# Kernel optimization log

Hardware: AMD Instinct MI355X
Metric: run time of the kernel (lower is better)

## Reference

```python
import jax, jax.numpy as jnp
import numpy as np

B, T, C, H, W = 16, 128, 32, 16, 16
NUM_FEAT = 16
D = C * H * W            # conv1d in-channels (kernel size 1 => linear)
G = NUM_FEAT * H * W     # G3 out-channels


def setup_inputs() -> dict:
    key = jax.random.key(0)
    ks = jax.random.split(key, 8)
    s1 = 1.0 / np.sqrt(D)
    return {
        "input1": jax.random.normal(ks[0], (B, T, C, H, W), jnp.float32),
        "input2": jax.random.normal(ks[1], (B, T, C, H, W), jnp.float32),
        "w1": jax.random.uniform(ks[2], (NUM_FEAT, D), jnp.float32, -s1, s1),
        "b1": jax.random.uniform(ks[3], (NUM_FEAT,), jnp.float32, -s1, s1),
        "w2": jax.random.uniform(ks[4], (NUM_FEAT, D), jnp.float32, -s1, s1),
        "b2": jax.random.uniform(ks[5], (NUM_FEAT,), jnp.float32, -s1, s1),
        "w3": jax.random.uniform(ks[6], (G, D), jnp.float32, -s1, s1),
        "b3": jax.random.uniform(ks[7], (G,), jnp.float32, -s1, s1),
    }


def reference(input1, input2, w1, b1, w2, b2, w3, b3):
    b, t = input1.shape[:2]
    x1 = input1.reshape(b, t, D)  # [B,T,D]
    x2 = input2.reshape(b, t, D)
    # Conv1d(kernel=1) projections (channels-first conv == per-frame linear)
    q = jnp.einsum('btd,fd->btf', x1, w1) + b1          # [B,T,F]
    k = jnp.einsum('bsd,fd->bsf', x2, w2) + b2          # [B,S,F]
    scores = jnp.einsum('btf,bsf->bts', q, k)            # [B,T,T]
    attn = jax.nn.softmax(scores, axis=1)                # softmax over dim=1 (rows)
    v = jnp.einsum('bsd,gd->bsg', x1, w3) + b3           # [B,T,G]
    out = jnp.einsum('bts,bsg->btg', attn, v)            # [B,T,G]
    return out.reshape(b, t, NUM_FEAT, H, W)
```

## Files before the change

### kernel.cpp

```cpp
#include <hip/hip_runtime.h>
#include <cstdint>
#include <cstddef>

#define Bn 16
#define Tn 128
#define Dn 8192
#define Fn 16
#define Gn 4096
#define MT (Bn*Tn)

typedef __attribute__((ext_vector_type(8))) short short8;
typedef __attribute__((ext_vector_type(4))) float f32x4;

__device__ inline short f2bf(float f) {
    union { float f; uint32_t u; } c; c.f = f;
    uint32_t u = c.u;
    uint32_t r = (u + 0x7FFFu + ((u >> 16) & 1u)) >> 16;
    return (short)(r & 0xFFFFu);
}

__device__ inline short8 cvt8(float4 a, float4 b) {
    short8 v;
    v[0] = f2bf(a.x); v[1] = f2bf(a.y); v[2] = f2bf(a.z); v[3] = f2bf(a.w);
    v[4] = f2bf(b.x); v[5] = f2bf(b.y); v[6] = f2bf(b.z); v[7] = f2bf(b.w);
    return v;
}

#define N8_X1 (MT * Dn / 8)
#define N8_W3 ((size_t)Gn * Dn / 8)

__global__ __launch_bounds__(256) void cvt2_kernel(
    const float* __restrict__ x1, const float* __restrict__ w3,
    short* __restrict__ x1b, short* __restrict__ w3b)
{
    const size_t total = N8_X1 + N8_W3;
    size_t i = (size_t)blockIdx.x * 256 + threadIdx.x;
    const size_t stride = (size_t)gridDim.x * 256;
    for (; i < total; i += stride) {
        if (i < N8_X1) {
            const float4* s = ((const float4*)x1) + i * 2;
            ((short8*)x1b)[i] = cvt8(s[0], s[1]);
        } else {
            const size_t j = i - N8_X1;
            const float4* s = ((const float4*)w3) + j * 2;
            ((short8*)w3b)[j] = cvt8(s[0], s[1]);
        }
    }
}

__global__ __launch_bounds__(256) void qk_gemm_kernel(
    const short* __restrict__ x1b, const float* __restrict__ x2,
    const float* __restrict__ w1, const float* __restrict__ w2,
    const float* __restrict__ b1, const float* __restrict__ b2,
    float* __restrict__ q, float* __restrict__ k)
{
    __shared__ float red[4][16][16];
    const int tid = threadIdx.x;
    const int tile = blockIdx.x >> 1;
    const int isK  = blockIdx.x & 1;
    const int m0 = tile * 16;
    const int wave = tid >> 6, lane = tid & 63;
    const int quad = lane >> 4, r = lane & 15;
    const int kbase = wave * (Dn / 4);

    f32x4 acc = {};

    if (!isK) {
        const short* ap = x1b + (size_t)(m0 + r) * Dn + kbase + quad * 8;
        const float* bp = w1 + (size_t)r * Dn + kbase + quad * 8;
        #pragma unroll 4
        for (int it = 0; it < 64; ++it) {
            short8 af = *(const short8*)(ap + it * 32);
            const float4* b4 = (const float4*)(bp + it * 32);
            short8 bf = cvt8(b4[0], b4[1]);
            acc = __builtin_amdgcn_mfma_f32_16x16x32_bf16(af, bf, acc, 0, 0, 0);
        }
    } else {
        const float* apf = x2 + (size_t)(m0 + r) * Dn + kbase + quad * 8;
        const float* bp  = w2 + (size_t)r * Dn + kbase + quad * 8;
        #pragma unroll 4
        for (int it = 0; it < 64; ++it) {
            const float4* a4 = (const float4*)(apf + it * 32);
            short8 af = cvt8(a4[0], a4[1]);
            const float4* b4 = (const float4*)(bp + it * 32);
            short8 bf = cvt8(b4[0], b4[1]);
            acc = __builtin_amdgcn_mfma_f32_16x16x32_bf16(af, bf, acc, 0, 0, 0);
        }
    }

    #pragma unroll
    for (int reg = 0; reg < 4; ++reg)
        red[wave][quad * 4 + reg][r] = acc[reg];
    __syncthreads();

    const int m = tid >> 4, f = tid & 15;
    float s = red[0][m][f] + red[1][m][f] + red[2][m][f] + red[3][m][f];
    s += (isK ? b2 : b1)[f];
    (isK ? k : q)[(m0 + m) * Fn + f] = s;
}

__global__ __launch_bounds__(128) void attn_kernel(
    const float* __restrict__ q, const float* __restrict__ k,
    short* __restrict__ attn16)
{
    __shared__ float qs[Tn * 17];
    const int b = blockIdx.x;
    const int tid = threadIdx.x;

    for (int i = tid; i < Tn * Fn; i += 128)
        qs[(i >> 4) * 17 + (i & 15)] = q[b * Tn * Fn + i];
    __syncthreads();

    float kr[16];
    #pragma unroll
    for (int f = 0; f < 16; ++f) kr[f] = k[b * Tn * Fn + tid * Fn + f];

    float m = -1e30f, sum = 0.f;
    #pragma unroll 1
    for (int t = 0; t < Tn; ++t) {
        float sc = 0.f;
        #pragma unroll
        for (int f = 0; f < 16; ++f) sc += qs[t * 17 + f] * kr[f];
        if (sc > m) { sum = sum * __expf(m - sc) + 1.f; m = sc; }
        else        { sum += __expf(sc - m); }
    }
    const float inv = 1.f / sum;
    short* ap = attn16 + (size_t)b * Tn * Tn;
    #pragma unroll 1
    for (int t = 0; t < Tn; ++t) {
        float sc = 0.f;
        #pragma unroll
        for (int f = 0; f < 16; ++f) sc += qs[t * 17 + f] * kr[f];
        ap[t * Tn + tid] = f2bf(__expf(sc - m) * inv);
    }
}

#define BK 32
#define KSPLIT 2
#define KHALF (Dn / KSPLIT)

__global__ __launch_bounds__(256) void gemm_v_split_kernel(
    const short* __restrict__ A, const short* __restrict__ Bw,
    float* __restrict__ vTf)
{
    __shared__ __attribute__((aligned(16))) short As[128 * BK];
    __shared__ __attribute__((aligned(16))) short Bs[128 * BK];

    const int tid = threadIdx.x;
    const int m0 = blockIdx.y * 128;
    const int n0 = blockIdx.x * 128;
    const int z  = blockIdx.z;
    const int kbase = z * KHALF;
    float* outp = vTf + (size_t)z * Gn * MT;
    const int wave = tid >> 6, lane = tid & 63;
    const int wm = (wave >> 1) * 64, wn = (wave & 1) * 64;
    const int quad = lane >> 4, r = lane & 15;

    const int srow = wave * 32 + (lane >> 2);
    const int scol = (lane & 3) * 8;
    const short* gA = A  + (size_t)(m0 + srow) * Dn + kbase + scol;
    const short* gB = Bw + (size_t)(n0 + srow) * Dn + kbase + scol;
    short* lA = &As[srow * BK + scol];
    short* lB = &Bs[srow * BK + scol];

    f32x4 acc[4][4] = {};

    #pragma unroll 1
    for (int k0 = 0; k0 < KHALF; k0 += BK) {
        __syncthreads();
        __builtin_amdgcn_global_load_lds(
            (const __attribute__((address_space(1))) void*)(gA + k0),
            (__attribute__((address_space(3))) void*)lA, 16, 0, 0);
        __builtin_amdgcn_global_load_lds(
            (const __attribute__((address_space(1))) void*)(gA + k0 + (size_t)16 * Dn),
            (__attribute__((address_space(3))) void*)(lA + 16 * BK), 16, 0, 0);
        __builtin_amdgcn_global_load_lds(
            (const __attribute__((address_space(1))) void*)(gB + k0),
            (__attribute__((address_space(3))) void*)lB, 16, 0, 0);
        __builtin_amdgcn_global_load_lds(
            (const __attribute__((address_space(1))) void*)(gB + k0 + (size_t)16 * Dn),
            (__attribute__((address_space(3))) void*)(lB + 16 * BK), 16, 0, 0);
        __syncthreads();

        short8 af[4], bf[4];
        #pragma unroll
        for (int i = 0; i < 4; ++i)
            af[i] = *(const short8*)&As[(wm + i * 16 + r) * BK + quad * 8];
        #pragma unroll
        for (int j = 0; j < 4; ++j)
            bf[j] = *(const short8*)&Bs[(wn + j * 16 + r) * BK + quad * 8];

        #pragma unroll
        for (int i = 0; i < 4; ++i)
            #pragma unroll
            for (int j = 0; j < 4; ++j)
                acc[i][j] = __builtin_amdgcn_mfma_f32_16x16x32_bf16(
                    af[i], bf[j], acc[i][j], 0, 0, 0);
    }

    #pragma unroll
    for (int i = 0; i < 4; ++i) {
        #pragma unroll
        for (int reg = 0; reg < 4; ++reg) {
            const int rowg = m0 + wm + i * 16 + quad * 4 + reg;
            #pragma unroll
            for (int j = 0; j < 4; ++j) {
                const int col = n0 + wn + j * 16 + r;
                outp[(size_t)rowg * MT + col] = acc[i][j][reg];
            }
        }
    }
}

__global__ __launch_bounds__(256) void vt_cvt_kernel(
    const float* __restrict__ vTf, const float* __restrict__ bias,
    short* __restrict__ vT)
{
    const size_t N8 = (size_t)Gn * MT / 8;
    const float4* p0 = (const float4*)vTf;
    const float4* p1 = (const float4*)(vTf + (size_t)Gn * MT);
    size_t i = (size_t)blockIdx.x * 256 + threadIdx.x;
    const size_t stride = (size_t)gridDim.x * 256;
    for (; i < N8; i += stride) {
        const float bv = bias[i >> 8];
        float4 a0 = p0[i * 2], b0 = p0[i * 2 + 1];
        float4 a1 = p1[i * 2], b1 = p1[i * 2 + 1];
        a0.x += a1.x + bv; a0.y += a1.y + bv; a0.z += a1.z + bv; a0.w += a1.w + bv;
        b0.x += b1.x + bv; b0.y += b1.y + bv; b0.z += b1.z + bv; b0.w += b1.w + bv;
        ((short8*)vT)[i] = cvt8(a0, b0);
    }
}

__global__ __launch_bounds__(256) void gemm_v_kernel(
    const short* __restrict__ A, const short* __restrict__ Bw,
    const float* __restrict__ bias, short* __restrict__ vT)
{
    __shared__ __attribute__((aligned(16))) short As[128 * BK];
    __shared__ __attribute__((aligned(16))) short Bs[128 * BK];

    const int tid = threadIdx.x;
    const int m0 = blockIdx.y * 128;
    const int n0 = blockIdx.x * 128;
    const int wave = tid >> 6, lane = tid & 63;
    const int wm = (wave >> 1) * 64, wn = (wave & 1) * 64;
    const int quad = lane >> 4, r = lane & 15;

    const int srow = wave * 32 + (lane >> 2);
    const int scol = (lane & 3) * 8;
    const short* gA = A  + (size_t)(m0 + srow) * Dn + scol;
    const short* gB = Bw + (size_t)(n0 + srow) * Dn + scol;
    short* lA = &As[srow * BK + scol];
    short* lB = &Bs[srow * BK + scol];

    f32x4 acc[4][4] = {};

    #pragma unroll 1
    for (int k0 = 0; k0 < Dn; k0 += BK) {
        __syncthreads();
        __builtin_amdgcn_global_load_lds(
            (const __attribute__((address_space(1))) void*)(gA + k0),
            (__attribute__((address_space(3))) void*)lA, 16, 0, 0);
        __builtin_amdgcn_global_load_lds(
            (const __attribute__((address_space(1))) void*)(gA + k0 + (size_t)16 * Dn),
            (__attribute__((address_space(3))) void*)(lA + 16 * BK), 16, 0, 0);
        __builtin_amdgcn_global_load_lds(
            (const __attribute__((address_space(1))) void*)(gB + k0),
            (__attribute__((address_space(3))) void*)lB, 16, 0, 0);
        __builtin_amdgcn_global_load_lds(
            (const __attribute__((address_space(1))) void*)(gB + k0 + (size_t)16 * Dn),
            (__attribute__((address_space(3))) void*)(lB + 16 * BK), 16, 0, 0);
        __syncthreads();

        short8 af[4], bf[4];
        #pragma unroll
        for (int i = 0; i < 4; ++i)
            af[i] = *(const short8*)&As[(wm + i * 16 + r) * BK + quad * 8];
        #pragma unroll
        for (int j = 0; j < 4; ++j)
            bf[j] = *(const short8*)&Bs[(wn + j * 16 + r) * BK + quad * 8];

        #pragma unroll
        for (int i = 0; i < 4; ++i)
            #pragma unroll
            for (int j = 0; j < 4; ++j)
                acc[i][j] = __builtin_amdgcn_mfma_f32_16x16x32_bf16(
                    af[i], bf[j], acc[i][j], 0, 0, 0);
    }

    #pragma unroll
    for (int i = 0; i < 4; ++i) {
        #pragma unroll
        for (int reg = 0; reg < 4; ++reg) {
            const int rowg = m0 + wm + i * 16 + quad * 4 + reg;
            const float bv = bias[rowg];
            #pragma unroll
            for (int j = 0; j < 4; ++j) {
                const int col = n0 + wn + j * 16 + r;
                vT[(size_t)rowg * MT + col] = f2bf(acc[i][j][reg] + bv);
            }
        }
    }
}

__global__ __launch_bounds__(256) void out_gemm_kernel(
    const short* __restrict__ attn16, const short* __restrict__ vT,
    float* __restrict__ out)
{
    __shared__ __attribute__((aligned(16))) short As[128 * BK];
    __shared__ __attribute__((aligned(16))) short Bs[128 * BK];

    const int tid = threadIdx.x;
    const int b  = blockIdx.y;
    const int n0 = blockIdx.x * 128;
    const int wave = tid >> 6, lane = tid & 63;
    const int wm = (wave >> 1) * 64, wn = (wave & 1) * 64;
    const int quad = lane >> 4, r = lane & 15;

    const int srow = wave * 32 + (lane >> 2);
    const int scol = (lane & 3) * 8;
    const short* gA = attn16 + (size_t)b * Tn * Tn + srow * Tn + scol;
    const short* gB = vT + (size_t)(n0 + srow) * MT + b * Tn + scol;
    short* lA = &As[srow * BK + scol];
    short* lB = &Bs[srow * BK + scol];

    f32x4 acc[4][4] = {};

    #pragma unroll 1
    for (int k0 = 0; k0 < Tn; k0 += BK) {
        __syncthreads();
        __builtin_amdgcn_global_load_lds(
            (const __attribute__((address_space(1))) void*)(gA + k0),
            (__attribute__((address_space(3))) void*)lA, 16, 0, 0);
        __builtin_amdgcn_global_load_lds(
            (const __attribute__((address_space(1))) void*)(gA + k0 + 16 * Tn),
            (__attribute__((address_space(3))) void*)(lA + 16 * BK), 16, 0, 0);
        __builtin_amdgcn_global_load_lds(
            (const __attribute__((address_space(1))) void*)(gB + k0),
            (__attribute__((address_space(3))) void*)lB, 16, 0, 0);
        __builtin_amdgcn_global_load_lds(
            (const __attribute__((address_space(1))) void*)(gB + k0 + (size_t)16 * MT),
            (__attribute__((address_space(3))) void*)(lB + 16 * BK), 16, 0, 0);
        __syncthreads();

        short8 af[4], bf[4];
        #pragma unroll
        for (int i = 0; i < 4; ++i)
            af[i] = *(const short8*)&As[(wm + i * 16 + r) * BK + quad * 8];
        #pragma unroll
        for (int j = 0; j < 4; ++j)
            bf[j] = *(const short8*)&Bs[(wn + j * 16 + r) * BK + quad * 8];

        #pragma unroll
        for (int i = 0; i < 4; ++i)
            #pragma unroll
            for (int j = 0; j < 4; ++j)
                acc[i][j] = __builtin_amdgcn_mfma_f32_16x16x32_bf16(
                    af[i], bf[j], acc[i][j], 0, 0, 0);
    }

    #pragma unroll
    for (int j = 0; j < 4; ++j) {
        const int col = n0 + wn + j * 16 + r;
        #pragma unroll
        for (int i = 0; i < 4; ++i) {
            #pragma unroll
            for (int reg = 0; reg < 4; ++reg) {
                const int rowt = wm + i * 16 + quad * 4 + reg;
                out[((size_t)(b * Tn + rowt)) * Gn + col] = acc[i][j][reg];
            }
        }
    }
}

extern "C" void kernel_launch(void* const* d_in, const int* in_sizes, int n_in,
                              void* d_out, int out_size, void* d_ws, size_t ws_size,
                              hipStream_t stream)
{
    const float* x1 = (const float*)d_in[0];
    const float* x2 = (const float*)d_in[1];
    const float* w1 = (const float*)d_in[2];
    const float* b1 = (const float*)d_in[3];
    const float* w2 = (const float*)d_in[4];
    const float* b2 = (const float*)d_in[5];
    const float* w3 = (const float*)d_in[6];
    const float* b3 = (const float*)d_in[7];
    float* out = (float*)d_out;

    float* q      = (float*)d_ws;
    float* k      = q + MT * Fn;
    short* attn16 = (short*)(k + MT * Fn);
    short* vT     = attn16 + (size_t)Bn * Tn * Tn;
    short* x1b    = vT + (size_t)Gn * MT;
    short* w3b    = x1b + (size_t)MT * Dn;
    float* vTf    = (float*)(w3b + (size_t)Gn * Dn);

    const size_t need_split =
        (size_t)MT * Fn * 4 * 2 +
        (size_t)Bn * Tn * Tn * 2 +
        (size_t)Gn * MT * 2 +
        (size_t)MT * Dn * 2 +
        (size_t)Gn * Dn * 2 +
        (size_t)KSPLIT * Gn * MT * 4;

    cvt2_kernel<<<4096, 256, 0, stream>>>(x1, w3, x1b, w3b);
    qk_gemm_kernel<<<256, 256, 0, stream>>>(x1b, x2, w1, w2, b1, b2, q, k);
    attn_kernel<<<Bn, 128, 0, stream>>>(q, k, attn16);

    if (ws_size >= need_split) {
        gemm_v_split_kernel<<<dim3(MT / 128, Gn / 128, KSPLIT), 256, 0, stream>>>(
            w3b, x1b, vTf);
        vt_cvt_kernel<<<2048, 256, 0, stream>>>(vTf, b3, vT);
    } else {
        gemm_v_kernel<<<dim3(MT / 128, Gn / 128), 256, 0, stream>>>(w3b, x1b, b3, vT);
    }

    out_gemm_kernel<<<dim3(Gn / 128, Bn), 256, 0, stream>>>(attn16, vT, out);
}
```

Before: 568.8 us.

## Parallelize attention softmax per column, raise V split-K, narrow output GEMM tiles

The attention kernel now gives each wave one key column and computes the column softmax with wave shuffles across 128 rows, launching Bn*32 blocks instead of 16 serial blocks. The V GEMM split-K becomes runtime-selectable, defaulting to 4 when the workspace allows, with the reduction kernel looping over the partial sums. The output GEMM uses 128x64 tiles to double the block count. The aim is more parallelism in small kernels, at the cost of more fp32 partial traffic in the split-K reduction.

```diff
diff --git a/kernel.cpp b/kernel.cpp
--- a/kernel.cpp
+++ b/kernel.cpp
@@ -99,49 +99,52 @@
     (isK ? k : q)[(m0 + m) * Fn + f] = s;
 }
 
-__global__ __launch_bounds__(128) void attn_kernel(
+__global__ __launch_bounds__(256) void attn_kernel(
     const float* __restrict__ q, const float* __restrict__ k,
     short* __restrict__ attn16)
 {
     __shared__ float qs[Tn * 17];
     const int b = blockIdx.x;
     const int tid = threadIdx.x;
-
-    for (int i = tid; i < Tn * Fn; i += 128)
+    const int wave = tid >> 6, lane = tid & 63;
+    const int s = blockIdx.y * 4 + wave;
+
+    for (int i = tid; i < Tn * Fn; i += 256)
         qs[(i >> 4) * 17 + (i & 15)] = q[b * Tn * Fn + i];
     __syncthreads();
 
     float kr[16];
     #pragma unroll
-    for (int f = 0; f < 16; ++f) kr[f] = k[b * Tn * Fn + tid * Fn + f];
-
-    float m = -1e30f, sum = 0.f;
-    #pragma unroll 1
-    for (int t = 0; t < Tn; ++t) {
-        float sc = 0.f;
-        #pragma unroll
-        for (int f = 0; f < 16; ++f) sc += qs[t * 17 + f] * kr[f];
-        if (sc > m) { sum = sum * __expf(m - sc) + 1.f; m = sc; }
-        else        { sum += __expf(sc - m); }
-    }
-    const float inv = 1.f / sum;
+    for (int f = 0; f < 16; ++f) kr[f] = k[((size_t)b * Tn + s) * Fn + f];
+
+    const int t0 = lane, t1 = lane + 64;
+    float sc0 = 0.f, sc1 = 0.f;
+    #pragma unroll
+    for (int f = 0; f < 16; ++f) {
+        sc0 += qs[t0 * 17 + f] * kr[f];
+        sc1 += qs[t1 * 17 + f] * kr[f];
+    }
+    float m = fmaxf(sc0, sc1);
+    #pragma unroll
+    for (int off = 32; off > 0; off >>= 1)
+        m = fmaxf(m, __shfl_xor(m, off, 64));
+    const float e0 = __expf(sc0 - m), e1 = __expf(sc1 - m);
+    float ssum = e0 + e1;
+    #pragma unroll
+    for (int off = 32; off > 0; off >>= 1)
+        ssum += __shfl_xor(ssum, off, 64);
+    const float inv = 1.f / ssum;
+
     short* ap = attn16 + (size_t)b * Tn * Tn;
-    #pragma unroll 1
-    for (int t = 0; t < Tn; ++t) {
-        float sc = 0.f;
-        #pragma unroll
-        for (int f = 0; f < 16; ++f) sc += qs[t * 17 + f] * kr[f];
-        ap[t * Tn + tid] = f2bf(__expf(sc - m) * inv);
-    }
+    ap[t0 * Tn + s] = f2bf(e0 * inv);
+    ap[t1 * Tn + s] = f2bf(e1 * inv);
 }
 
 #define BK 32
-#define KSPLIT 2
-#define KHALF (Dn / KSPLIT)
 
 __global__ __launch_bounds__(256) void gemm_v_split_kernel(
     const short* __restrict__ A, const short* __restrict__ Bw,
-    float* __restrict__ vTf)
+    float* __restrict__ vTf, const int kspan)
 {
     __shared__ __attribute__((aligned(16))) short As[128 * BK];
     __shared__ __attribute__((aligned(16))) short Bs[128 * BK];
@@ -150,7 +153,7 @@
     const int m0 = blockIdx.y * 128;
     const int n0 = blockIdx.x * 128;
     const int z  = blockIdx.z;
-    const int kbase = z * KHALF;
+    const int kbase = z * kspan;
     float* outp = vTf + (size_t)z * Gn * MT;
     const int wave = tid >> 6, lane = tid & 63;
     const int wm = (wave >> 1) * 64, wn = (wave & 1) * 64;
@@ -166,7 +169,7 @@
     f32x4 acc[4][4] = {};
 
     #pragma unroll 1
-    for (int k0 = 0; k0 < KHALF; k0 += BK) {
+    for (int k0 = 0; k0 < kspan; k0 += BK) {
         __syncthreads();
         __builtin_amdgcn_global_load_lds(
             (const __attribute__((address_space(1))) void*)(gA + k0),
@@ -214,20 +217,21 @@
 
 __global__ __launch_bounds__(256) void vt_cvt_kernel(
     const float* __restrict__ vTf, const float* __restrict__ bias,
-    short* __restrict__ vT)
+    short* __restrict__ vT, const int nparts)
 {
     const size_t N8 = (size_t)Gn * MT / 8;
-    const float4* p0 = (const float4*)vTf;
-    const float4* p1 = (const float4*)(vTf + (size_t)Gn * MT);
     size_t i = (size_t)blockIdx.x * 256 + threadIdx.x;
     const size_t stride = (size_t)gridDim.x * 256;
     for (; i < N8; i += stride) {
         const float bv = bias[i >> 8];
-        float4 a0 = p0[i * 2], b0 = p0[i * 2 + 1];
-        float4 a1 = p1[i * 2], b1 = p1[i * 2 + 1];
-        a0.x += a1.x + bv; a0.y += a1.y + bv; a0.z += a1.z + bv; a0.w += a1.w + bv;
-        b0.x += b1.x + bv; b0.y += b1.y + bv; b0.z += b1.z + bv; b0.w += b1.w + bv;
-        ((short8*)vT)[i] = cvt8(a0, b0);
+        float4 a = {bv, bv, bv, bv}, b = {bv, bv, bv, bv};
+        for (int p = 0; p < nparts; ++p) {
+            const float4* pp = (const float4*)(vTf + (size_t)p * Gn * MT);
+            float4 a1 = pp[i * 2], b1 = pp[i * 2 + 1];
+            a.x += a1.x; a.y += a1.y; a.z += a1.z; a.w += a1.w;
+            b.x += b1.x; b.y += b1.y; b.z += b1.z; b.w += b1.w;
+        }
+        ((short8*)vT)[i] = cvt8(a, b);
     }
 }
 
@@ -307,23 +311,24 @@
     float* __restrict__ out)
 {
     __shared__ __attribute__((aligned(16))) short As[128 * BK];
-    __shared__ __attribute__((aligned(16))) short Bs[128 * BK];
+    __shared__ __attribute__((aligned(16))) short Bs[64 * BK];
 
     const int tid = threadIdx.x;
     const int b  = blockIdx.y;
-    const int n0 = blockIdx.x * 128;
+    const int n0 = blockIdx.x * 64;
     const int wave = tid >> 6, lane = tid & 63;
-    const int wm = (wave >> 1) * 64, wn = (wave & 1) * 64;
+    const int wm = (wave >> 1) * 64, wn = (wave & 1) * 32;
     const int quad = lane >> 4, r = lane & 15;
 
-    const int srow = wave * 32 + (lane >> 2);
+    const int srowA = wave * 32 + (lane >> 2);
+    const int srowB = wave * 16 + (lane >> 2);
     const int scol = (lane & 3) * 8;
-    const short* gA = attn16 + (size_t)b * Tn * Tn + srow * Tn + scol;
-    const short* gB = vT + (size_t)(n0 + srow) * MT + b * Tn + scol;
-    short* lA = &As[srow * BK + scol];
-    short* lB = &Bs[srow * BK + scol];
-
-    f32x4 acc[4][4] = {};
+    const short* gA = attn16 + (size_t)b * Tn * Tn + srowA * Tn + scol;
+    const short* gB = vT + (size_t)(n0 + srowB) * MT + b * Tn + scol;
+    short* lA = &As[srowA * BK + scol];
+    short* lB = &Bs[srowB * BK + scol];
+
+    f32x4 acc[4][2] = {};
 
     #pragma unroll 1
     for (int k0 = 0; k0 < Tn; k0 += BK) {
@@ -337,29 +342,26 @@
         __builtin_amdgcn_global_load_lds(
             (const __attribute__((address_space(1))) void*)(gB + k0),
             (__attribute__((address_space(3))) void*)lB, 16, 0, 0);
-        __builtin_amdgcn_global_load_lds(
-            (const __attribute__((address_space(1))) void*)(gB + k0 + (size_t)16 * MT),
-            (__attribute__((address_space(3))) void*)(lB + 16 * BK), 16, 0, 0);
-        __syncthreads();
-
-        short8 af[4], bf[4];
+        __syncthreads();
+
+        short8 af[4], bf[2];
         #pragma unroll
         for (int i = 0; i < 4; ++i)
             af[i] = *(const short8*)&As[(wm + i * 16 + r) * BK + quad * 8];
         #pragma unroll
-        for (int j = 0; j < 4; ++j)
+        for (int j = 0; j < 2; ++j)
             bf[j] = *(const short8*)&Bs[(wn + j * 16 + r) * BK + quad * 8];
 
         #pragma unroll
         for (int i = 0; i < 4; ++i)
             #pragma unroll
-            for (int j = 0; j < 4; ++j)
+            for (int j = 0; j < 2; ++j)
                 acc[i][j] = __builtin_amdgcn_mfma_f32_16x16x32_bf16(
                     af[i], bf[j], acc[i][j], 0, 0, 0);
     }
 
     #pragma unroll
-    for (int j = 0; j < 4; ++j) {
+    for (int j = 0; j < 2; ++j) {
         const int col = n0 + wn + j * 16 + r;
         #pragma unroll
         for (int i = 0; i < 4; ++i) {
@@ -394,25 +396,29 @@
     short* w3b    = x1b + (size_t)MT * Dn;
     float* vTf    = (float*)(w3b + (size_t)Gn * Dn);
 
-    const size_t need_split =
+    const size_t base_need =
         (size_t)MT * Fn * 4 * 2 +
         (size_t)Bn * Tn * Tn * 2 +
         (size_t)Gn * MT * 2 +
         (size_t)MT * Dn * 2 +
-        (size_t)Gn * Dn * 2 +
-        (size_t)KSPLIT * Gn * MT * 4;
+        (size_t)Gn * Dn * 2;
+    const size_t psize = (size_t)Gn * MT * 4;
+
+    int ksplit = 0;
+    if (ws_size >= base_need + 4 * psize)      ksplit = 4;
+    else if (ws_size >= base_need + 2 * psize) ksplit = 2;
 
     cvt2_kernel<<<4096, 256, 0, stream>>>(x1, w3, x1b, w3b);
     qk_gemm_kernel<<<256, 256, 0, stream>>>(x1b, x2, w1, w2, b1, b2, q, k);
-    attn_kernel<<<Bn, 128, 0, stream>>>(q, k, attn16);
-
-    if (ws_size >= need_split) {
-        gemm_v_split_kernel<<<dim3(MT / 128, Gn / 128, KSPLIT), 256, 0, stream>>>(
-            w3b, x1b, vTf);
-        vt_cvt_kernel<<<2048, 256, 0, stream>>>(vTf, b3, vT);
+    attn_kernel<<<dim3(Bn, Tn / 4), 256, 0, stream>>>(q, k, attn16);
+
+    if (ksplit) {
+        gemm_v_split_kernel<<<dim3(MT / 128, Gn / 128, ksplit), 256, 0, stream>>>(
+            w3b, x1b, vTf, Dn / ksplit);
+        vt_cvt_kernel<<<2048, 256, 0, stream>>>(vTf, b3, vT, ksplit);
     } else {
         gemm_v_kernel<<<dim3(MT / 128, Gn / 128), 256, 0, stream>>>(w3b, x1b, b3, vT);
     }
 
-    out_gemm_kernel<<<dim3(Gn / 128, Bn), 256, 0, stream>>>(attn16, vT, out);
-}
+    out_gemm_kernel<<<dim3(Gn / 64, Bn), 256, 0, stream>>>(attn16, vT, out);
+}
```

Result: faster. 548.9 us (-3.5%).
